# Optimization experiments

Measured on AMD Instinct MI355X. Metric: run time of the kernel, lower is better.

The kernel has to match this reference:

```python
import jax, jax.numpy as jnp
import numpy as np

CHEB_K = 3  # matches init_kwargs


def setup_inputs() -> dict:
    key = jax.random.key(0)
    k1, k2, k3, k4 = jax.random.split(key, 4)
    B, N, C_IN, C_OUT, D = 64, 4000, 64, 64, 10
    x = jax.random.normal(k1, (B, N, C_IN), dtype=jnp.float32)
    node_emb = jax.random.normal(k2, (N, D), dtype=jnp.float32)
    weights_pool = jax.random.normal(k3, (D, CHEB_K, C_IN, C_OUT), dtype=jnp.float32) * 0.1
    bias_pool = jax.random.normal(k4, (D, C_OUT), dtype=jnp.float32) * 0.1
    return {"x": x, "node_emb": node_emb, "weights_pool": weights_pool, "bias_pool": bias_pool}


def reference(x, node_emb, weights_pool, bias_pool):
    # adpadj == 'agcrn': adaptive adjacency from node embeddings
    N = node_emb.shape[0]
    supports = jax.nn.softmax(jax.nn.relu(node_emb @ node_emb.T), axis=1)  # [N,N]
    # Chebyshev polynomial basis: T0=I, T1=A, Tk = 2A Tk-1 - Tk-2
    support_set = [jnp.eye(N, dtype=x.dtype), supports]
    for _ in range(2, CHEB_K):
        support_set.append(2.0 * supports @ support_set[-1] - support_set[-2])
    S = jnp.stack(support_set, axis=0)  # [K,N,N]
    # per-node generated weights and bias
    weights = jnp.einsum('nd,dkio->nkio', node_emb, weights_pool)  # [N,K,Cin,Cout]
    bias = node_emb @ bias_pool  # [N,Cout]
    # graph conv: aggregate neighbors for each Chebyshev order, then per-node matmul
    x_g = jnp.einsum('knm,bmc->bnkc', S, x)  # [B,N,K,Cin]
    out = jnp.einsum('bnki,nkio->bno', x_g, weights) + bias  # [B,N,Cout]
    return out
```

## Files before the change

### kernel.cpp

```cpp
#include <hip/hip_runtime.h>

typedef __attribute__((ext_vector_type(8))) __bf16 bf16x8;
typedef __attribute__((ext_vector_type(4))) float f32x4;
typedef __attribute__((ext_vector_type(8))) unsigned short u16x8;

#define N_NODES 4000
#define LD 4096
#define KDIM 4000
#define D_EMB 10

__device__ __forceinline__ unsigned short f2bf(float f) {
  union { float f; unsigned int u; } v; v.f = f;
  unsigned int r = v.u + 0x7fffu + ((v.u >> 16) & 1u);
  return (unsigned short)(r >> 16);
}
__device__ __forceinline__ float bf2f(unsigned short s) {
  union { unsigned int u; float f; } v; v.u = ((unsigned int)s) << 16;
  return v.f;
}

#define AS1 __attribute__((address_space(1)))
#define AS3 __attribute__((address_space(3)))
__device__ __forceinline__ void gll16(const void* g, void* l) {
  __builtin_amdgcn_global_load_lds((const AS1 void*)g, (AS3 void*)l, 16, 0, 0);
}

__global__ __launch_bounds__(256) void transpose_x_kernel(const float* __restrict__ x,
                                                          unsigned short* __restrict__ Xc) {
  __shared__ float tl[64 * 65];
  const int t = threadIdx.x;
  const int m0 = blockIdx.x * 64;
  const int b = blockIdx.y;
#pragma unroll
  for (int rep = 0; rep < 16; ++rep) {
    int idx = rep * 256 + t;
    int ml = idx >> 6, c = idx & 63;
    int m = m0 + ml;
    tl[ml * 65 + c] = (m < N_NODES) ? x[(b * N_NODES + m) * 64 + c] : 0.f;
  }
  __syncthreads();
  const int c_out = t >> 2, q = t & 3;
  u16x8 v0, v1;
#pragma unroll
  for (int j = 0; j < 8; ++j) v0[j] = f2bf(tl[(q * 16 + j) * 65 + c_out]);
#pragma unroll
  for (int j = 0; j < 8; ++j) v1[j] = f2bf(tl[(q * 16 + 8 + j) * 65 + c_out]);
  unsigned short* dst = Xc + (size_t)(b * 64 + c_out) * LD + m0 + q * 16;
  *(u16x8*)dst = v0;
  *(u16x8*)(dst + 8) = v1;
}

__global__ __launch_bounds__(256) void build_adj_kernel(const float* __restrict__ emb,
                                                        unsigned short* __restrict__ A) {
  __shared__ float e_lds[N_NODES];
  __shared__ float embn[16];
  __shared__ float red[16];
  const int n = blockIdx.x, t = threadIdx.x;
  if (t < D_EMB) embn[t] = emb[n * D_EMB + t];
  __syncthreads();
  float lsum = 0.f;
  for (int m = t; m < N_NODES; m += 256) {
    float dot = 0.f;
#pragma unroll
    for (int d = 0; d < D_EMB; ++d) dot += embn[d] * emb[m * D_EMB + d];
    float e = __expf(fmaxf(dot, 0.f));
    e_lds[m] = e;
    lsum += e;
  }
#pragma unroll
  for (int off = 32; off > 0; off >>= 1) lsum += __shfl_down(lsum, off, 64);
  const int lane = t & 63, wave = t >> 6;
  if (lane == 0) red[wave] = lsum;
  __syncthreads();
  if (t == 0) red[8] = 1.f / (red[0] + red[1] + red[2] + red[3]);
  __syncthreads();
  const float inv = red[8];
  for (int m = t; m < LD; m += 256) {
    float v = (m < N_NODES) ? e_lds[m] * inv : 0.f;
    A[(size_t)n * LD + m] = f2bf(v);
  }
}

__global__ __launch_bounds__(256) void wp_cvt_kernel(const float* __restrict__ wp,
                                                     unsigned short* __restrict__ wpb) {
  int i = blockIdx.x * 256 + threadIdx.x;
  if (i < D_EMB * 12288) wpb[i] = f2bf(wp[i]);
}

template <bool WRITE_T>
__global__ __launch_bounds__(256, 4) void gemm_bt_kernel(const unsigned short* __restrict__ Amat,
                                                         const unsigned short* __restrict__ Bmat,
                                                         unsigned short* __restrict__ Cn,
                                                         unsigned short* __restrict__ Ct) {
  __shared__ __align__(16) char smem[WRITE_T ? (128 * 136 * 2) : (2 * 128 * 32 * 2)];
  unsigned short* At = (unsigned short*)smem;
  unsigned short* Bt = At + 128 * 32;
  const int tid = threadIdx.x;
  const int wave = tid >> 6, lane = tid & 63;
  const int bm = blockIdx.y * 128, bn = blockIdx.x * 128;
  const int wm = (wave >> 1) * 64, wn = (wave & 1) * 64;

  const unsigned short* gA = Amat + (size_t)(bm + wave * 32 + (lane >> 2)) * LD + (lane & 3) * 8;
  const unsigned short* gB = Bmat + (size_t)(bn + wave * 32 + (lane >> 2)) * LD + (lane & 3) * 8;
  char* lA0 = smem + wave * 2048;
  char* lA1 = lA0 + 1024;
  char* lB0 = smem + 8192 + wave * 2048;
  char* lB1 = lB0 + 1024;

  f32x4 acc[4][4] = {};
  const unsigned short* Ap = At + (wm + (lane & 15)) * 32 + (lane >> 4) * 8;
  const unsigned short* Bp = Bt + (wn + (lane & 15)) * 32 + (lane >> 4) * 8;

  for (int kt = 0; kt < KDIM / 32; ++kt) {
    gll16(gA, lA0);
    gll16(gA + 16 * LD, lA1);
    gll16(gB, lB0);
    gll16(gB + 16 * LD, lB1);
    gA += 32; gB += 32;
    __syncthreads();
    bf16x8 af[4], bfr[4];
#pragma unroll
    for (int i = 0; i < 4; ++i) {
      af[i] = *(const bf16x8*)(Ap + i * 512);
      bfr[i] = *(const bf16x8*)(Bp + i * 512);
    }
#pragma unroll
    for (int mt = 0; mt < 4; ++mt)
#pragma unroll
      for (int nt = 0; nt < 4; ++nt)
        acc[mt][nt] = __builtin_amdgcn_mfma_f32_16x16x32_bf16(af[mt], bfr[nt], acc[mt][nt], 0, 0, 0);
    __syncthreads();
  }

#pragma unroll
  for (int mt = 0; mt < 4; ++mt)
#pragma unroll
    for (int nt = 0; nt < 4; ++nt)
#pragma unroll
      for (int r = 0; r < 4; ++r) {
        int row = bm + wm + mt * 16 + (lane >> 4) * 4 + r;
        int col = bn + wn + nt * 16 + (lane & 15);
        Cn[(size_t)row * LD + col] = f2bf(acc[mt][nt][r]);
      }

  if (WRITE_T) {
    unsigned short* tr = (unsigned short*)smem;
    __syncthreads();
#pragma unroll
    for (int mt = 0; mt < 4; ++mt)
#pragma unroll
      for (int nt = 0; nt < 4; ++nt)
#pragma unroll
        for (int r = 0; r < 4; ++r) {
          int row = wm + mt * 16 + (lane >> 4) * 4 + r;
          int col = wn + nt * 16 + (lane & 15);
          tr[col * 136 + row] = f2bf(acc[mt][nt][r]);
        }
    __syncthreads();
    const int cl = tid >> 1, half = tid & 1;
    const unsigned short* src = tr + cl * 136 + half * 64;
    unsigned short* dst = Ct + (size_t)(bn + cl) * LD + bm + half * 64;
#pragma unroll
    for (int j = 0; j < 8; ++j)
      *(u16x8*)(dst + j * 8) = *(const u16x8*)(src + j * 8);
  }
}

#define EST 200
__global__ __launch_bounds__(256) void epilogue_kernel(const float* __restrict__ x,
                                                       const float* __restrict__ emb,
                                                       const unsigned short* __restrict__ wpb,
                                                       const float* __restrict__ bp,
                                                       const unsigned short* __restrict__ Y1,
                                                       const unsigned short* __restrict__ Y2,
                                                       float* __restrict__ out) {
  __shared__ unsigned short Wt[64 * EST];
  __shared__ unsigned short xg[64 * EST];
  __shared__ float embn[16];
  const int n = blockIdx.x, t = threadIdx.x;
  if (t < D_EMB) embn[t] = emb[n * D_EMB + t];
  __syncthreads();
#pragma unroll 4
  for (int rep = 0; rep < 48; ++rep) {
    int kio = rep * 256 + t;
    int ki = kio >> 6, o = kio & 63;
    float a = 0.f;
#pragma unroll
    for (int d = 0; d < D_EMB; ++d) a += embn[d] * bf2f(wpb[d * 12288 + kio]);
    Wt[o * EST + ki] = f2bf(a);
  }
  for (int idx = t; idx < 4096; idx += 256) {
    int b = idx >> 6, c = idx & 63;
    xg[b * EST + c] = f2bf(x[(size_t)(b * N_NODES + n) * 64 + c]);
  }
  for (int idx = t; idx < 4096; idx += 256) {
    int b = idx >> 6, c = idx & 63;
    xg[b * EST + 64 + c] = Y1[(size_t)n * LD + b * 64 + c];
  }
  for (int idx = t; idx < 4096; idx += 256) {
    int b = idx >> 6, c = idx & 63;
    float v = 2.f * bf2f(Y2[(size_t)n * LD + b * 64 + c]) - bf2f(xg[b * EST + c]);
    xg[b * EST + 128 + c] = f2bf(v);
  }
  __syncthreads();

  const int wave = t >> 6, lane = t & 63, quad = lane >> 4;
  const unsigned short* Apx = xg + (wave * 16 + (lane & 15)) * EST + quad * 8;
  f32x4 acc[4] = {};
#pragma unroll
  for (int step = 0; step < 6; ++step) {
    int koff = step * 32;
    bf16x8 a = *(const bf16x8*)(Apx + koff);
#pragma unroll
    for (int nt = 0; nt < 4; ++nt) {
      bf16x8 bfr = *(const bf16x8*)(Wt + (nt * 16 + (lane & 15)) * EST + quad * 8 + koff);
      acc[nt] = __builtin_amdgcn_mfma_f32_16x16x32_bf16(a, bfr, acc[nt], 0, 0, 0);
    }
  }
  float bias[4];
#pragma unroll
  for (int nt = 0; nt < 4; ++nt) {
    float a = 0.f;
#pragma unroll
    for (int d = 0; d < D_EMB; ++d) a += embn[d] * bp[d * 64 + nt * 16 + (lane & 15)];
    bias[nt] = a;
  }
#pragma unroll
  for (int nt = 0; nt < 4; ++nt)
#pragma unroll
    for (int rr = 0; rr < 4; ++rr) {
      int b_row = wave * 16 + quad * 4 + rr;
      out[(size_t)(b_row * N_NODES + n) * 64 + nt * 16 + (lane & 15)] = acc[nt][rr] + bias[nt];
    }
}

extern "C" void kernel_launch(void* const* d_in, const int* in_sizes, int n_in,
                              void* d_out, int out_size, void* d_ws, size_t ws_size,
                              hipStream_t stream) {
  const float* x   = (const float*)d_in[0];
  const float* emb = (const float*)d_in[1];
  const float* wp  = (const float*)d_in[2];
  const float* bp  = (const float*)d_in[3];
  float* out = (float*)d_out;

  unsigned short* Xc  = (unsigned short*)d_ws;
  unsigned short* Am  = Xc  + (size_t)LD * LD;
  unsigned short* Y1  = Am  + (size_t)LD * LD;
  unsigned short* Y1t = Y1  + (size_t)LD * LD;
  unsigned short* Y2  = Y1t + (size_t)LD * LD;
  unsigned short* wpb = Xc;

  transpose_x_kernel<<<dim3(63, 64), 256, 0, stream>>>(x, Xc);
  build_adj_kernel<<<N_NODES, 256, 0, stream>>>(emb, Am);
  gemm_bt_kernel<true ><<<dim3(32, 32), 256, 0, stream>>>(Am, Xc, Y1, Y1t);
  wp_cvt_kernel<<<480, 256, 0, stream>>>(wp, wpb);
  gemm_bt_kernel<false><<<dim3(32, 32), 256, 0, stream>>>(Am, Y1t, Y2, nullptr);
  epilogue_kernel<<<N_NODES, 256, 0, stream>>>(x, emb, wpb, bp, Y1, Y2, out);
}
```

Baseline: 575.1 us.

## Precompute per-node weights in separate kernel and vectorize epilogue loads

Adds a transposing bf16 conversion of weights_pool and a wgen kernel that materializes all per-node weight matrices into the workspace in the layout the epilogue wants. The epilogue then copies its weight tile with 16-byte loads instead of recomputing it from the pool with scattered reads. The x, Y1 and Y2 staging loops are vectorized. The cost is an extra round trip of roughly 100 MB through global memory, and the workspace buffers are reordered so the new buffer can reuse the space of dead intermediates.

```diff
diff --git a/kernel.cpp b/kernel.cpp
--- a/kernel.cpp
+++ b/kernel.cpp
@@ -3,6 +3,7 @@
 typedef __attribute__((ext_vector_type(8))) __bf16 bf16x8;
 typedef __attribute__((ext_vector_type(4))) float f32x4;
 typedef __attribute__((ext_vector_type(8))) unsigned short u16x8;
+typedef __attribute__((ext_vector_type(4))) unsigned short u16x4;
 
 #define N_NODES 4000
 #define LD 4096
@@ -81,10 +82,45 @@
   }
 }
 
-__global__ __launch_bounds__(256) void wp_cvt_kernel(const float* __restrict__ wp,
-                                                     unsigned short* __restrict__ wpb) {
-  int i = blockIdx.x * 256 + threadIdx.x;
-  if (i < D_EMB * 12288) wpb[i] = f2bf(wp[i]);
+__global__ __launch_bounds__(256) void wpt_kernel(const float* __restrict__ wp,
+                                                  unsigned short* __restrict__ wpT) {
+  __shared__ float tl[64 * 65];
+  const int dk = blockIdx.x;
+  const int d = dk / 3, k = dk % 3;
+  const float* src = wp + (size_t)dk * 4096;
+  const int t = threadIdx.x;
+#pragma unroll
+  for (int rep = 0; rep < 16; ++rep) {
+    int idx = rep * 256 + t;
+    tl[(idx >> 6) * 65 + (idx & 63)] = src[idx];
+  }
+  __syncthreads();
+#pragma unroll
+  for (int rep = 0; rep < 16; ++rep) {
+    int idx = rep * 256 + t;
+    int o = idx >> 6, i = idx & 63;
+    wpT[(size_t)d * 12288 + o * 192 + k * 64 + i] = f2bf(tl[i * 65 + o]);
+  }
+}
+
+__global__ __launch_bounds__(256) void wgen_kernel(const float* __restrict__ emb,
+                                                   const unsigned short* __restrict__ wpT,
+                                                   unsigned short* __restrict__ W_all) {
+  __shared__ float el[50 * D_EMB];
+  const int t = threadIdx.x;
+  const int j = blockIdx.x * 256 + t;
+  const int n0 = blockIdx.y * 50;
+  for (int idx = t; idx < 50 * D_EMB; idx += 256) el[idx] = emb[n0 * D_EMB + idx];
+  __syncthreads();
+  float w[D_EMB];
+#pragma unroll
+  for (int d = 0; d < D_EMB; ++d) w[d] = bf2f(wpT[(size_t)d * 12288 + j]);
+  for (int n = 0; n < 50; ++n) {
+    float a = 0.f;
+#pragma unroll
+    for (int d = 0; d < D_EMB; ++d) a += el[n * D_EMB + d] * w[d];
+    W_all[(size_t)(n0 + n) * 12288 + j] = f2bf(a);
+  }
 }
 
 template <bool WRITE_T>
@@ -169,7 +205,7 @@
 #define EST 200
 __global__ __launch_bounds__(256) void epilogue_kernel(const float* __restrict__ x,
                                                        const float* __restrict__ emb,
-                                                       const unsigned short* __restrict__ wpb,
+                                                       const unsigned short* __restrict__ W_all,
                                                        const float* __restrict__ bp,
                                                        const unsigned short* __restrict__ Y1,
                                                        const unsigned short* __restrict__ Y2,
@@ -179,28 +215,36 @@
   __shared__ float embn[16];
   const int n = blockIdx.x, t = threadIdx.x;
   if (t < D_EMB) embn[t] = emb[n * D_EMB + t];
-  __syncthreads();
-#pragma unroll 4
-  for (int rep = 0; rep < 48; ++rep) {
-    int kio = rep * 256 + t;
-    int ki = kio >> 6, o = kio & 63;
-    float a = 0.f;
-#pragma unroll
-    for (int d = 0; d < D_EMB; ++d) a += embn[d] * bf2f(wpb[d * 12288 + kio]);
-    Wt[o * EST + ki] = f2bf(a);
-  }
-  for (int idx = t; idx < 4096; idx += 256) {
-    int b = idx >> 6, c = idx & 63;
-    xg[b * EST + c] = f2bf(x[(size_t)(b * N_NODES + n) * 64 + c]);
-  }
-  for (int idx = t; idx < 4096; idx += 256) {
-    int b = idx >> 6, c = idx & 63;
-    xg[b * EST + 64 + c] = Y1[(size_t)n * LD + b * 64 + c];
-  }
-  for (int idx = t; idx < 4096; idx += 256) {
-    int b = idx >> 6, c = idx & 63;
-    float v = 2.f * bf2f(Y2[(size_t)n * LD + b * 64 + c]) - bf2f(xg[b * EST + c]);
-    xg[b * EST + 128 + c] = f2bf(v);
+
+  {
+    const int o = t >> 2, sub = t & 3;
+    const unsigned short* srcW = W_all + (size_t)n * 12288 + o * 192 + sub * 48;
+    unsigned short* dstW = Wt + o * EST + sub * 48;
+#pragma unroll
+    for (int c = 0; c < 6; ++c)
+      *(u16x8*)(dstW + c * 8) = *(const u16x8*)(srcW + c * 8);
+  }
+  for (int idx = t; idx < 1024; idx += 256) {
+    int b = idx >> 4, c4 = (idx & 15) * 4;
+    f32x4 v = *(const f32x4*)(x + (size_t)(b * N_NODES + n) * 64 + c4);
+    u16x4 s;
+#pragma unroll
+    for (int j = 0; j < 4; ++j) s[j] = f2bf(v[j]);
+    *(u16x4*)(xg + b * EST + c4) = s;
+  }
+  for (int idx = t; idx < 512; idx += 256) {
+    int b = idx >> 3, c8 = (idx & 7) * 8;
+    *(u16x8*)(xg + b * EST + 64 + c8) = *(const u16x8*)(Y1 + (size_t)n * LD + b * 64 + c8);
+  }
+  __syncthreads();
+  for (int idx = t; idx < 512; idx += 256) {
+    int b = idx >> 3, c8 = (idx & 7) * 8;
+    u16x8 y2 = *(const u16x8*)(Y2 + (size_t)n * LD + b * 64 + c8);
+    u16x8 r;
+#pragma unroll
+    for (int j = 0; j < 8; ++j)
+      r[j] = f2bf(2.f * bf2f(y2[j]) - bf2f(xg[b * EST + c8 + j]));
+    *(u16x8*)(xg + b * EST + 128 + c8) = r;
   }
   __syncthreads();
 
@@ -243,17 +287,20 @@
   const float* bp  = (const float*)d_in[3];
   float* out = (float*)d_out;
 
-  unsigned short* Xc  = (unsigned short*)d_ws;
-  unsigned short* Am  = Xc  + (size_t)LD * LD;
-  unsigned short* Y1  = Am  + (size_t)LD * LD;
-  unsigned short* Y1t = Y1  + (size_t)LD * LD;
-  unsigned short* Y2  = Y1t + (size_t)LD * LD;
-  unsigned short* wpb = Xc;
+  const size_t S = (size_t)LD * LD;
+  unsigned short* Y1    = (unsigned short*)d_ws;
+  unsigned short* Y2    = Y1 + S;
+  unsigned short* Xc    = Y1 + 2 * S;
+  unsigned short* Am    = Y1 + 3 * S;
+  unsigned short* Y1t   = Y1 + 4 * S;
+  unsigned short* wpT   = Xc;
+  unsigned short* W_all = Xc + 256 * 1024;
 
   transpose_x_kernel<<<dim3(63, 64), 256, 0, stream>>>(x, Xc);
   build_adj_kernel<<<N_NODES, 256, 0, stream>>>(emb, Am);
   gemm_bt_kernel<true ><<<dim3(32, 32), 256, 0, stream>>>(Am, Xc, Y1, Y1t);
-  wp_cvt_kernel<<<480, 256, 0, stream>>>(wp, wpb);
   gemm_bt_kernel<false><<<dim3(32, 32), 256, 0, stream>>>(Am, Y1t, Y2, nullptr);
-  epilogue_kernel<<<N_NODES, 256, 0, stream>>>(x, emb, wpb, bp, Y1, Y2, out);
-}
+  wpt_kernel<<<30, 256, 0, stream>>>(wp, wpT);
+  wgen_kernel<<<dim3(48, 80), 256, 0, stream>>>(emb, wpT, W_all);
+  epilogue_kernel<<<N_NODES, 256, 0, stream>>>(x, emb, W_all, bp, Y1, Y2, out);
+}
```

Result: faster. 555.5 us (-3.4%).
